# Kernel optimization log

Measured on AMD Instinct MI355X. Metric: run time of the kernel, lower is better.

Reference implementation:

```python
import jax, jax.numpy as jnp
import numpy as np
from jax import lax

EPS = 1e-5
B, C, H, W = 16, 256, 56, 56
HEADS, DIM_K, DIM_U, DIM_OUT = 4, 16, 4, 256
DIM_V = DIM_OUT // HEADS  # 64
R = 15


def setup_inputs() -> dict:
    key = jax.random.key(0)
    ks = jax.random.split(key, 16)
    s = 0.05
    return {
        "x": jax.random.normal(ks[0], (B, C, H, W), jnp.float32),
        "Wq": jax.random.normal(ks[1], (C, HEADS * DIM_K), jnp.float32) * s,
        "Wk": jax.random.normal(ks[2], (C, DIM_U * DIM_K), jnp.float32) * s,
        "Wv": jax.random.normal(ks[3], (C, DIM_U * DIM_V), jnp.float32) * s,
        "pos_w": jax.random.normal(ks[4], (DIM_K, DIM_U, 1, R, R), jnp.float32) * s,
        "pos_b": jax.random.normal(ks[5], (DIM_K,), jnp.float32) * s,
        "gq": jax.random.uniform(ks[6], (HEADS * DIM_K,), jnp.float32),
        "bq": jax.random.normal(ks[7], (HEADS * DIM_K,), jnp.float32) * s,
        "mq": jax.random.normal(ks[8], (HEADS * DIM_K,), jnp.float32) * s,
        "vq": jax.random.uniform(ks[9], (HEADS * DIM_K,), jnp.float32) + 0.5,
        "gv": jax.random.uniform(ks[10], (DIM_U * DIM_V,), jnp.float32),
        "bv": jax.random.normal(ks[11], (DIM_U * DIM_V,), jnp.float32) * s,
        "mv": jax.random.normal(ks[12], (DIM_U * DIM_V,), jnp.float32) * s,
        "vv": jax.random.uniform(ks[13], (DIM_U * DIM_V,), jnp.float32) + 0.5,
    }


def _bn(x, gamma, beta, mean, var):
    # inference-mode BatchNorm over channel dim (axis=1), x: [b,c,h,w]
    inv = gamma / jnp.sqrt(var + EPS)
    return x * inv[None, :, None, None] + (beta - mean * inv)[None, :, None, None]


def reference(x, Wq, Wk, Wv, pos_w, pos_b, gq, bq, mq, vq, gv, bv, mv, vv):
    b, c, hh, ww = x.shape
    n = hh * ww
    h, dk, u, dv = HEADS, DIM_K, DIM_U, DIM_V
    # 1x1 convs (channels_first) == channel matmuls
    q = jnp.einsum('bchw,cd->bdhw', x, Wq)
    k = jnp.einsum('bchw,cd->bdhw', x, Wk)
    v = jnp.einsum('bchw,cd->bdhw', x, Wv)
    q = _bn(q, gq, bq, mq, vq)
    v = _bn(v, gv, bv, mv, vv)
    # rearranges: 'b (h k) hh ww -> b h k (hh ww)', 'b (u k) hh ww -> b u k n', 'b (u v) hh ww -> b u v n'
    q = q.reshape(b, h, dk, n)
    k = k.reshape(b, u, dk, n)
    v = v.reshape(b, u, dv, n)
    k = jax.nn.softmax(k, axis=-1)  # keras Softmax default axis=-1 (positions)
    # content lambda
    Lc = jnp.einsum('bukm,buvm->bkv', k, v)
    Yc = jnp.einsum('bhkn,bkv->bnhv', q, Lc)
    # position lambda: conv3d over (v,hh,ww) with kernel (1,r,r), pad spatial only
    v5 = v.reshape(b, u, dv, hh, ww)  # [N, C=u, D=v, H, W]
    p = R // 2
    Lp = lax.conv_general_dilated(
        v5, pos_w, window_strides=(1, 1, 1),
        padding=[(0, 0), (p, p), (p, p)],
        dimension_numbers=('NCDHW', 'OIDHW', 'NCDHW'))
    Lp = Lp + pos_b[None, :, None, None, None]  # [b, k, v, hh, ww]
    Lp = Lp.reshape(b, dk, dv, n)
    Yp = jnp.einsum('bhkn,bkvn->bnhv', q, Lp)
    Y = Yc + Yp  # [b, n, h, v]
    # 'b (hh ww) h v -> b (h v) hh ww'
    out = Y.reshape(b, hh, ww, h, dv).transpose(0, 3, 4, 1, 2).reshape(b, h * dv, hh, ww)
    return out
```

## Files before the change

kernel.cpp:

```cpp
#include <hip/hip_runtime.h>
#include <cstdint>
#include <cstddef>

#define NB   16
#define NC   256
#define NPIX 3136
#define NW   56
#define EPSV 1e-5f

#define BSTR   (384 * NPIX)
#define OFF_VP (128 * NPIX)
#define VROWD  36
#define VPLANE (56 * VROWD)

#define OFF_AB   0u
#define OFF_BNA  49152u
#define OFF_BNB  49536u
#define OFF_WT   49920u
#define OFF_KS   58112u
#define OFF_LC   59136u
#define OFF_Y    75520u

typedef short bf16x8 __attribute__((ext_vector_type(8)));
typedef float f32x4  __attribute__((ext_vector_type(4)));
typedef float f32x16 __attribute__((ext_vector_type(16)));

__device__ __forceinline__ uint32_t f2bf(float f) {
  uint32_t x = __float_as_uint(f);
  uint32_t r = x + 0x7fffu + ((x >> 16) & 1u);
  return r >> 16;
}
__device__ __forceinline__ uint32_t pk_trunc(float a, float b) {
  return (__float_as_uint(a) >> 16) | (__float_as_uint(b) & 0xffff0000u);
}

__device__ __forceinline__ float fetchW(const float* Wq, const float* Wk,
                                        const float* Wv, int m, int c) {
  if (m < 64)  return Wq[c * 64 + m];
  if (m < 128) return Wk[c * 64 + (m - 64)];
  return Wv[c * 256 + (m - 128)];
}

__global__ void prep_kernel(const float* __restrict__ Wq, const float* __restrict__ Wk,
                            const float* __restrict__ Wv, const float* __restrict__ pos_w,
                            const float* __restrict__ gq, const float* __restrict__ bq,
                            const float* __restrict__ mq, const float* __restrict__ vq,
                            const float* __restrict__ gv, const float* __restrict__ bv,
                            const float* __restrict__ mv, const float* __restrict__ vv,
                            float* __restrict__ ws) {
  int d = blockIdx.x;
  int c = threadIdx.x;
  int i = d * 256 + c;
  if (i < 49152) {
    int dgt = i >> 12, rem = i & 4095;
    int kc = rem >> 8, rem2 = rem & 255;
    int lane = rem2 >> 2, dp = rem2 & 3;
    int m = dgt * 32 + (lane & 31);
    int k0 = kc * 16 + (lane >> 5) * 8 + dp * 2;
    float w0 = fetchW(Wq, Wk, Wv, m, k0);
    float w1 = fetchW(Wq, Wk, Wv, m, k0 + 1);
    ((uint32_t*)(ws + OFF_AB))[i] = f2bf(w0) | (f2bf(w1) << 16);
  }
  if (c == 0) {
    float sa, sb;
    if (d < 64)        { float inv = gq[d] / sqrtf(vq[d] + EPSV); sa = inv; sb = bq[d] - mq[d] * inv; }
    else if (d < 128)  { sa = 1.0f; sb = 0.0f; }
    else               { int j = d - 128; float inv = gv[j] / sqrtf(vv[j] + EPSV); sa = inv; sb = bv[j] - mv[j] * inv; }
    ws[OFF_BNA + d] = sa;
    ws[OFF_BNB + d] = sb;
  }
  if (i < 8192) {
    int chunk = i >> 8, rem = i & 255, lane = rem >> 2, dp = rem & 3;
    int quad = lane >> 4, k = lane & 15;
    int u = chunk >> 3, t = chunk & 7;
    int dh = 2 * t + (quad >> 1);
    int dwb = (quad & 1) * 8 + dp * 2;
    float w0 = (dh < 15 && dwb     < 15) ? pos_w[k * 900 + u * 225 + dh * 15 + dwb]     : 0.0f;
    float w1 = (dh < 15 && dwb + 1 < 15) ? pos_w[k * 900 + u * 225 + dh * 15 + dwb + 1] : 0.0f;
    ((uint32_t*)(ws + OFF_WT))[i] = f2bf(w0) | (f2bf(w1) << 16);
  }
  if (i < 1024) ws[OFF_KS + i] = 0.0f;
  for (int g = i; g < 4096 * 56; g += 98304) {
    int plane = g / 56, r = g - plane * 56;
    int bb = plane >> 8, d2 = plane & 255;
    uint32_t* row = (uint32_t*)(ws + OFF_Y) + (size_t)bb * BSTR + OFF_VP
                    + (size_t)d2 * VPLANE + r * VROWD;
    uint4 z; z.x = 0; z.y = 0; z.z = 0; z.w = 0;
    *(uint4*)(row)      = z;
    *(uint4*)(row + 32) = z;
  }
}

__launch_bounds__(256, 2)
__global__ void qkv_mfma(const float* __restrict__ x, const float* __restrict__ wsc,
                         float* __restrict__ Y) {
  __shared__ uint32_t X[64 * 128];
  __shared__ float BNs[768];
  int tid = threadIdx.x;
  int n0 = blockIdx.x * 64, b = blockIdx.y;
  for (int i = tid; i < 768; i += 256) BNs[i] = wsc[OFF_BNA + i];
  const size_t xb = (size_t)b * NC * NPIX;
#pragma unroll
  for (int it = 0; it < 4; ++it) {
    int n2 = tid & 31;
    int cp4 = it * 8 + (tid >> 5);
    const float* xp = x + xb + (size_t)(cp4 * 8) * NPIX + n0 + n2 * 2;
    float2 ld[8];
#pragma unroll
    for (int j = 0; j < 8; ++j) ld[j] = *(const float2*)(xp + (size_t)j * NPIX);
    uint32_t e0, e1, e2, e3, o0, o1, o2, o3;
    e0 = f2bf(ld[0].x) | (f2bf(ld[1].x) << 16);
    e1 = f2bf(ld[2].x) | (f2bf(ld[3].x) << 16);
    e2 = f2bf(ld[4].x) | (f2bf(ld[5].x) << 16);
    e3 = f2bf(ld[6].x) | (f2bf(ld[7].x) << 16);
    o0 = f2bf(ld[0].y) | (f2bf(ld[1].y) << 16);
    o1 = f2bf(ld[2].y) | (f2bf(ld[3].y) << 16);
    o2 = f2bf(ld[4].y) | (f2bf(ld[5].y) << 16);
    o3 = f2bf(ld[6].y) | (f2bf(ld[7].y) << 16);
    int ne = 2 * n2, no = ne + 1;
    uint4 ve; ve.x = e0; ve.y = e1; ve.z = e2; ve.w = e3;
    uint4 vo; vo.x = o0; vo.y = o1; vo.z = o2; vo.w = o3;
    *(uint4*)(X + ne * 128 + ((cp4 ^ (ne & 31)) << 2)) = ve;
    *(uint4*)(X + no * 128 + ((cp4 ^ (no & 31)) << 2)) = vo;
  }
  __syncthreads();
  int lane = tid & 63, w = tid >> 6;
  int n31 = lane & 31, h5 = lane >> 5;
  f32x16 acc[3][2];
#pragma unroll
  for (int dt = 0; dt < 3; ++dt)
#pragma unroll
    for (int nt = 0; nt < 2; ++nt)
#pragma unroll
      for (int e = 0; e < 16; ++e) acc[dt][nt][e] = 0.0f;
  const uint4* AB = (const uint4*)(wsc + OFF_AB);
#pragma unroll 4
  for (int kc = 0; kc < 16; ++kc) {
    bf16x8 af[3];
#pragma unroll
    for (int dt = 0; dt < 3; ++dt) {
      union { uint4 q; bf16x8 v; } tmp;
      tmp.q = AB[(size_t)(((w * 3 + dt) * 16 + kc)) * 64 + lane];
      af[dt] = tmp.v;
    }
#pragma unroll
    for (int nt = 0; nt < 2; ++nt) {
      union { uint4 q; bf16x8 v; } bu;
      bu.q = *(const uint4*)(X + (nt * 32 + n31) * 128 + (((2 * kc + h5) ^ n31) << 2));
#pragma unroll
      for (int dt = 0; dt < 3; ++dt)
        acc[dt][nt] = __builtin_amdgcn_mfma_f32_32x32x16_bf16(af[dt], bu.v, acc[dt][nt], 0, 0, 0);
    }
  }
#pragma unroll
  for (int dt = 0; dt < 3; ++dt) {
    int dgt = w * 3 + dt;
    float sa[16], sb[16];
#pragma unroll
    for (int g = 0; g < 4; ++g) {
      *(float4*)(sa + g * 4) = *(const float4*)(BNs + dgt * 32 + g * 8 + h5 * 4);
      *(float4*)(sb + g * 4) = *(const float4*)(BNs + 384 + dgt * 32 + g * 8 + h5 * 4);
    }
#pragma unroll
    for (int nt = 0; nt < 2; ++nt) {
      int pix = n0 + nt * 32 + n31;
      if (dgt < 2) {
        uint2* qb2 = (uint2*)(Y + (size_t)b * BSTR);
#pragma unroll
        for (int g = 0; g < 4; ++g) {
          float y0 = fmaf(acc[dt][nt][4 * g + 0], sa[4 * g + 0], sb[4 * g + 0]);
          float y1 = fmaf(acc[dt][nt][4 * g + 1], sa[4 * g + 1], sb[4 * g + 1]);
          float y2 = fmaf(acc[dt][nt][4 * g + 2], sa[4 * g + 2], sb[4 * g + 2]);
          float y3 = fmaf(acc[dt][nt][4 * g + 3], sa[4 * g + 3], sb[4 * g + 3]);
          uint2 val;
          val.x = f2bf(y0) | (f2bf(y1) << 16);
          val.y = f2bf(y2) | (f2bf(y3) << 16);
          qb2[(size_t)(dgt * 8 + 2 * g + h5) * NPIX + pix] = val;
        }
      } else if (dgt < 4) {
#pragma unroll
        for (int g = 0; g < 4; ++g)
#pragma unroll
          for (int ki = 0; ki < 4; ++ki) {
            int d = dgt * 32 + 8 * g + 4 * h5 + ki;
            Y[((size_t)b * 384 + d) * NPIX + pix] =
                fmaf(acc[dt][nt][4 * g + ki], sa[4 * g + ki], sb[4 * g + ki]);
          }
      } else {
        int pr = pix / NW, pc = pix - pr * NW;
        int ridx = pr * 72 + 8 + pc;
        unsigned short* vp = (unsigned short*)(Y + (size_t)b * BSTR + OFF_VP);
#pragma unroll
        for (int g = 0; g < 4; ++g)
#pragma unroll
          for (int ki = 0; ki < 4; ++ki) {
            int d2 = dgt * 32 + 8 * g + 4 * h5 + ki - 128;
            float yv = fmaf(acc[dt][nt][4 * g + ki], sa[4 * g + ki], sb[4 * g + ki]);
            vp[(size_t)d2 * 4032 + ridx] = (unsigned short)f2bf(yv);
          }
      }
    }
  }
}

__launch_bounds__(256)
__global__ void lc_mfma(float* __restrict__ Y, float* __restrict__ ws) {
  __shared__ float R[4096];
  __shared__ float Rs[64];
  int bx = blockIdx.x, u = blockIdx.y, b = blockIdx.z;
  int tid = threadIdx.x;
  int lane = tid & 63, w = tid >> 6;
  int col = lane & 15, quad = lane >> 4;
  int slot = bx * 4 + w;
  const float* krow = Y + ((size_t)(b * 384 + 64 + u * 16 + col)) * NPIX;
  const uint32_t* vpb = (const uint32_t*)(Y + (size_t)b * BSTR + OFF_VP)
                        + (size_t)(u * 64 + col) * VPLANE;
  f32x4 acc[4];
#pragma unroll
  for (int vt = 0; vt < 4; ++vt) acc[vt] = (f32x4){0.f, 0.f, 0.f, 0.f};
  float ssum = 0.0f;
  for (int c = slot; c < 126; c += 64) {
    int p0 = c * 32 + quad * 8;
    int row = p0 / 72;
    int pc = p0 - row * 72;
    bool valid = (unsigned)(pc - 8) < 56u;
    float4 k0, k1;
    if (valid) {
      const float* kp = krow + row * NW + pc - 8;
      k0 = *(const float4*)(kp);
      k1 = *(const float4*)(kp + 4);
    } else {
      k0.x = k0.y = k0.z = k0.w = -1e30f;
      k1 = k0;
    }
    float e0 = __expf(k0.x), e1 = __expf(k0.y), e2 = __expf(k0.z), e3 = __expf(k0.w);
    float e4 = __expf(k1.x), e5 = __expf(k1.y), e6 = __expf(k1.z), e7 = __expf(k1.w);
    ssum += (e0 + e1 + e2 + e3) + (e4 + e5 + e6 + e7);
    union { uint32_t d[4]; bf16x8 v; } kb;
    kb.d[0] = pk_trunc(e0, e1);
    kb.d[1] = pk_trunc(e2, e3);
    kb.d[2] = pk_trunc(e4, e5);
    kb.d[3] = pk_trunc(e6, e7);
    int vdw = c * 16 + quad * 4;
#pragma unroll
    for (int vt = 0; vt < 4; ++vt) {
      union { uint4 q; bf16x8 v; } vb;
      vb.q = *(const uint4*)(vpb + (size_t)(vt * 16) * VPLANE + vdw);
      acc[vt] = __builtin_amdgcn_mfma_f32_16x16x32_bf16(vb.v, kb.v, acc[vt], 0, 0, 0);
    }
  }
  ssum += __shfl_xor(ssum, 16);
  ssum += __shfl_xor(ssum, 32);
#pragma unroll
  for (int vt = 0; vt < 4; ++vt)
#pragma unroll
    for (int r = 0; r < 4; ++r)
      R[w * 1024 + vt * 256 + quad * 64 + r * 16 + col] = acc[vt][r];
  if (lane < 16) Rs[w * 16 + col] = ssum;
  __syncthreads();
  float* P = Y + (size_t)b * BSTR + 32 * NPIX + (size_t)(u * 16 + bx) * 1024;
  float4 s0 = *(const float4*)(R + tid * 4);
  float4 s1 = *(const float4*)(R + 1024 + tid * 4);
  float4 s2 = *(const float4*)(R + 2048 + tid * 4);
  float4 s3 = *(const float4*)(R + 3072 + tid * 4);
  float4 tot;
  tot.x = (s0.x + s1.x) + (s2.x + s3.x);
  tot.y = (s0.y + s1.y) + (s2.y + s3.y);
  tot.z = (s0.z + s1.z) + (s2.z + s3.z);
  tot.w = (s0.w + s1.w) + (s2.w + s3.w);
  *(float4*)(P + tid * 4) = tot;
  if (tid < 16)
    atomicAdd(&ws[OFF_KS + b * 64 + u * 16 + tid],
              (Rs[tid] + Rs[16 + tid]) + (Rs[32 + tid] + Rs[48 + tid]));
}

__global__ void lc_reduce(const float* __restrict__ Y, float* __restrict__ ws) {
  int i = blockIdx.x, b = blockIdx.y;
  int t = threadIdx.x;
  __shared__ float invS[64];
  if (t < 64) invS[t] = 1.0f / ws[OFF_KS + b * 64 + t];
  __syncthreads();
  int idx = i * 256 + t;
  int k = idx & 15;
  const float* P = Y + (size_t)b * BSTR + 32 * NPIX;
  float tot = 0.0f;
#pragma unroll
  for (int u = 0; u < 4; ++u) {
    float su = 0.0f;
#pragma unroll
    for (int s = 0; s < 16; ++s) su += P[(size_t)(u * 16 + s) * 1024 + idx];
    tot += su * invS[u * 16 + k];
  }
  ws[OFF_LC + (b * 16 + k) * 64 + (idx >> 4)] = tot;
}

#define ROWS    29
#define RSTR2   72
#define UPITCH2 2088
#define LDSW2   8352

__launch_bounds__(512, 4)
__global__ void pos_lambda_mfma(const float* __restrict__ Y, const float* __restrict__ wsc,
                                const float* __restrict__ pos_b, float* __restrict__ out) {
  __shared__ __attribute__((aligned(16))) uint32_t S[LDSW2];
  int v = blockIdx.x, b = blockIdx.y, band = blockIdx.z;
  int rb = band * 14;
  int tid = threadIdx.x;
  const uint32_t* vpad = (const uint32_t*)(Y + (size_t)b * BSTR + OFF_VP);
  for (int ii = tid; ii < 1044; ii += 512) {
    int u = ii / 261;
    int rem = ii - u * 261;
    int row = rem / 9;
    int j3 = rem - row * 9;
    int gr = rb + row - 7;
    uint32_t d0 = 0, d1 = 0, d2 = 0, d3 = 0, d4 = 0;
    if ((unsigned)gr < (unsigned)NW) {
      const uint32_t* pr32 = vpad + (size_t)(u * 64 + v) * VPLANE + gr * VROWD + 4 * j3;
      d0 = pr32[0]; d1 = pr32[1]; d2 = pr32[2]; d3 = pr32[3]; d4 = pr32[4];
    }
    uint32_t* dst = S + u * UPITCH2 + row * RSTR2 + 8 * j3;
    uint4 w0, w1;
    w0.x = __builtin_amdgcn_alignbit(d1, d0, 16);  w0.y = d1;
    w0.z = __builtin_amdgcn_alignbit(d2, d1, 16);  w0.w = d2;
    w1.x = __builtin_amdgcn_alignbit(d3, d2, 16);  w1.y = d3;
    w1.z = __builtin_amdgcn_alignbit(d4, d3, 16);  w1.w = d4;
    *(uint4*)(dst)     = w0;
    *(uint4*)(dst + 4) = w1;
  }
  __syncthreads();
  int lane = tid & 63, wid = tid >> 6;
  int quad = lane >> 4, n = lane & 15;
  int dhp = quad >> 1;
  int ct = wid & 3, p = wid >> 2;
  int cb = (ct == 3) ? 40 : ct * 16;
  int sb = cb + n + (quad & 1) * 8;
  int abase = (p + dhp) * RSTR2 + sb;
  const uint4* wt = (const uint4*)(wsc + OFF_WT);
  float lcq[4];
#pragma unroll
  for (int r = 0; r < 4; ++r) {
    int k = quad * 4 + r;
    lcq[r] = wsc[OFF_LC + (b * 16 + k) * 64 + v] + pos_b[k];
  }
  f32x4 acc[7];
#pragma unroll
  for (int q = 0; q < 7; ++q) {
    acc[q][0] = lcq[0]; acc[q][1] = lcq[1]; acc[q][2] = lcq[2]; acc[q][3] = lcq[3];
  }
#pragma unroll 1
  for (int u = 0; u < 4; ++u) {
    bf16x8 wf[8];
#pragma unroll
    for (int t = 0; t < 8; ++t) {
      union { uint4 q; bf16x8 v; } tmp;
      tmp.q = wt[(u * 8 + t) * 64 + lane];
      wf[t] = tmp.v;
    }
    int au = u * UPITCH2 + abase;
#pragma unroll
    for (int PP = 0; PP < 14; ++PP) {
      int a = au + PP * (2 * RSTR2);
      union { uint32_t u4[4]; bf16x8 v8; } bu;
      bu.u4[0] = S[a];     bu.u4[1] = S[a + 2];
      bu.u4[2] = S[a + 4]; bu.u4[3] = S[a + 6];
#pragma unroll
      for (int t = 0; t < 8; ++t) {
        int q = PP - t;
        if (q >= 0 && q < 7)
          acc[q] = __builtin_amdgcn_mfma_f32_16x16x32_bf16(wf[t], bu.v8, acc[q], 0, 0, 0);
      }
    }
  }
  const uint2* qb2 = (const uint2*)(Y + (size_t)b * BSTR);
#pragma unroll
  for (int q = 0; q < 7; ++q) {
    int rr = rb + p + 2 * q;
    int pix = rr * NW + cb + n;
    float m0 = acc[q][0], m1 = acc[q][1];
    float m2 = acc[q][2], m3 = acc[q][3];
    float pp[4];
#pragma unroll
    for (int j = 0; j < 4; ++j) {
      int h = quad ^ j;
      uint2 qd = qb2[(h * 4 + quad) * NPIX + pix];
      float q0 = __uint_as_float(qd.x << 16);
      float q1 = __uint_as_float(qd.x & 0xffff0000u);
      float q2 = __uint_as_float(qd.y << 16);
      float q3 = __uint_as_float(qd.y & 0xffff0000u);
      pp[j] = fmaf(q0, m0, fmaf(q1, m1, fmaf(q2, m2, q3 * m3)));
    }
    float t0 = pp[0] + __shfl_xor(pp[1], 16);
    float t2 = pp[2] + __shfl_xor(pp[3], 16);
    float y  = t0 + __shfl_xor(t2, 32);
    out[((size_t)(b * 256 + quad * 64 + v)) * NPIX + pix] = y;
  }
}

extern "C" void kernel_launch(void* const* d_in, const int* in_sizes, int n_in,
                              void* d_out, int out_size, void* d_ws, size_t ws_size,
                              hipStream_t stream) {
  const float* x     = (const float*)d_in[0];
  const float* Wq    = (const float*)d_in[1];
  const float* Wk    = (const float*)d_in[2];
  const float* Wv    = (const float*)d_in[3];
  const float* pos_w = (const float*)d_in[4];
  const float* pos_b = (const float*)d_in[5];
  const float* gq    = (const float*)d_in[6];
  const float* bq    = (const float*)d_in[7];
  const float* mq    = (const float*)d_in[8];
  const float* vq    = (const float*)d_in[9];
  const float* gv    = (const float*)d_in[10];
  const float* bv    = (const float*)d_in[11];
  const float* mv    = (const float*)d_in[12];
  const float* vv    = (const float*)d_in[13];
  float* ws  = (float*)d_ws;
  float* out = (float*)d_out;
  float* Y   = ws + OFF_Y;

  prep_kernel<<<dim3(384), 256, 0, stream>>>(Wq, Wk, Wv, pos_w, gq, bq, mq, vq,
                                             gv, bv, mv, vv, ws);
  qkv_mfma<<<dim3(49, 16), 256, 0, stream>>>(x, ws, Y);
  lc_mfma<<<dim3(16, 4, 16), 256, 0, stream>>>(Y, ws);
  lc_reduce<<<dim3(4, 16), 256, 0, stream>>>(Y, ws);
  pos_lambda_mfma<<<dim3(64, 16, 4), 512, 0, stream>>>(Y, ws, pos_b, out);
}
```

Measured before the change: 261.1 us.

## Split LDS tile into parity planes, skip padded-row MFMAs and duplicate stores

The position-lambda kernel now stages each input row in shared memory as two planes: an aligned copy and a half-word-shifted copy. Each B fragment can then be read from four consecutive words instead of four words at stride two. The MFMA loop also skips row pairs that fall entirely in the zero padding at the top and bottom bands. The overlapping last column tile no longer writes its duplicated pixels. The global load becomes a single 16-byte read, and the shared-memory footprint grows slightly, which could press on occupancy at four blocks per CU.

Result: slower. 291.6 us (+11.7%).

```diff
diff --git a/kernel.cpp b/kernel.cpp
--- a/kernel.cpp
+++ b/kernel.cpp
@@ -295,14 +295,15 @@
 }
 
 #define ROWS    29
-#define RSTR2   72
-#define UPITCH2 2088
-#define LDSW2   8352
+#define RSTR3   80
+#define P1OFF   44
+#define UPITCH3 2320
+#define LDSW3   9280
 
 __launch_bounds__(512, 4)
 __global__ void pos_lambda_mfma(const float* __restrict__ Y, const float* __restrict__ wsc,
                                 const float* __restrict__ pos_b, float* __restrict__ out) {
-  __shared__ __attribute__((aligned(16))) uint32_t S[LDSW2];
+  __shared__ __attribute__((aligned(16))) uint32_t S[LDSW3];
   int v = blockIdx.x, b = blockIdx.y, band = blockIdx.z;
   int rb = band * 14;
   int tid = threadIdx.x;
@@ -311,21 +312,24 @@
     int u = ii / 261;
     int rem = ii - u * 261;
     int row = rem / 9;
-    int j3 = rem - row * 9;
+    int j = rem - row * 9;
     int gr = rb + row - 7;
     uint32_t d0 = 0, d1 = 0, d2 = 0, d3 = 0, d4 = 0;
     if ((unsigned)gr < (unsigned)NW) {
-      const uint32_t* pr32 = vpad + (size_t)(u * 64 + v) * VPLANE + gr * VROWD + 4 * j3;
-      d0 = pr32[0]; d1 = pr32[1]; d2 = pr32[2]; d3 = pr32[3]; d4 = pr32[4];
-    }
-    uint32_t* dst = S + u * UPITCH2 + row * RSTR2 + 8 * j3;
-    uint4 w0, w1;
-    w0.x = __builtin_amdgcn_alignbit(d1, d0, 16);  w0.y = d1;
-    w0.z = __builtin_amdgcn_alignbit(d2, d1, 16);  w0.w = d2;
-    w1.x = __builtin_amdgcn_alignbit(d3, d2, 16);  w1.y = d3;
-    w1.z = __builtin_amdgcn_alignbit(d4, d3, 16);  w1.w = d4;
-    *(uint4*)(dst)     = w0;
-    *(uint4*)(dst + 4) = w1;
+      const uint32_t* pr = vpad + (size_t)(u * 64 + v) * VPLANE + gr * VROWD + 4 * j;
+      uint4 q4 = *(const uint4*)pr;
+      d0 = q4.x; d1 = q4.y; d2 = q4.z; d3 = q4.w;
+      d4 = pr[4];
+    }
+    uint32_t* dst = S + u * UPITCH3 + row * RSTR3 + 4 * j;
+    uint4 a4; a4.x = d0; a4.y = d1; a4.z = d2; a4.w = d3;
+    *(uint4*)(dst) = a4;
+    uint4 b4;
+    b4.x = __builtin_amdgcn_alignbit(d1, d0, 16);
+    b4.y = __builtin_amdgcn_alignbit(d2, d1, 16);
+    b4.z = __builtin_amdgcn_alignbit(d3, d2, 16);
+    b4.w = __builtin_amdgcn_alignbit(d4, d3, 16);
+    *(uint4*)(dst + P1OFF) = b4;
   }
   __syncthreads();
   int lane = tid & 63, wid = tid >> 6;
@@ -333,8 +337,11 @@
   int dhp = quad >> 1;
   int ct = wid & 3, p = wid >> 2;
   int cb = (ct == 3) ? 40 : ct * 16;
-  int sb = cb + n + (quad & 1) * 8;
-  int abase = (p + dhp) * RSTR2 + sb;
+  int s = cb + n + ((quad & 1) << 3) + 1;
+  int par = s & 1, sidx = s >> 1;
+  int base = (p + dhp) * RSTR3 + (par ? P1OFF : 0) + sidx;
+  int lo = (7 - rb) > 0 ? (7 - rb) : 0;
+  int hi = (63 - rb) < ROWS ? (63 - rb) : ROWS;
   const uint4* wt = (const uint4*)(wsc + OFF_WT);
   float lcq[4];
 #pragma unroll
@@ -356,13 +363,16 @@
       tmp.q = wt[(u * 8 + t) * 64 + lane];
       wf[t] = tmp.v;
     }
-    int au = u * UPITCH2 + abase;
+    const uint32_t* Sp = S + u * UPITCH3 + base;
 #pragma unroll
     for (int PP = 0; PP < 14; ++PP) {
-      int a = au + PP * (2 * RSTR2);
+      int r0 = p + 2 * PP;
+      if (r0 + 1 < lo || r0 >= hi) continue;
       union { uint32_t u4[4]; bf16x8 v8; } bu;
-      bu.u4[0] = S[a];     bu.u4[1] = S[a + 2];
-      bu.u4[2] = S[a + 4]; bu.u4[3] = S[a + 6];
+      bu.u4[0] = Sp[PP * 160];
+      bu.u4[1] = Sp[PP * 160 + 1];
+      bu.u4[2] = Sp[PP * 160 + 2];
+      bu.u4[3] = Sp[PP * 160 + 3];
 #pragma unroll
       for (int t = 0; t < 8; ++t) {
         int q = PP - t;
@@ -371,28 +381,31 @@
       }
     }
   }
-  const uint2* qb2 = (const uint2*)(Y + (size_t)b * BSTR);
-#pragma unroll
-  for (int q = 0; q < 7; ++q) {
-    int rr = rb + p + 2 * q;
-    int pix = rr * NW + cb + n;
-    float m0 = acc[q][0], m1 = acc[q][1];
-    float m2 = acc[q][2], m3 = acc[q][3];
-    float pp[4];
-#pragma unroll
-    for (int j = 0; j < 4; ++j) {
-      int h = quad ^ j;
-      uint2 qd = qb2[(h * 4 + quad) * NPIX + pix];
-      float q0 = __uint_as_float(qd.x << 16);
-      float q1 = __uint_as_float(qd.x & 0xffff0000u);
-      float q2 = __uint_as_float(qd.y << 16);
-      float q3 = __uint_as_float(qd.y & 0xffff0000u);
-      pp[j] = fmaf(q0, m0, fmaf(q1, m1, fmaf(q2, m2, q3 * m3)));
-    }
-    float t0 = pp[0] + __shfl_xor(pp[1], 16);
-    float t2 = pp[2] + __shfl_xor(pp[3], 16);
-    float y  = t0 + __shfl_xor(t2, 32);
-    out[((size_t)(b * 256 + quad * 64 + v)) * NPIX + pix] = y;
+  bool dup = (ct == 3) && (n < 8);
+  if (!dup) {
+    const uint2* qb2 = (const uint2*)(Y + (size_t)b * BSTR);
+#pragma unroll
+    for (int q = 0; q < 7; ++q) {
+      int rr = rb + p + 2 * q;
+      int pix = rr * NW + cb + n;
+      float m0 = acc[q][0], m1 = acc[q][1];
+      float m2 = acc[q][2], m3 = acc[q][3];
+      float pp[4];
+#pragma unroll
+      for (int j = 0; j < 4; ++j) {
+        int h = quad ^ j;
+        uint2 qd = qb2[(h * 4 + quad) * NPIX + pix];
+        float q0 = __uint_as_float(qd.x << 16);
+        float q1 = __uint_as_float(qd.x & 0xffff0000u);
+        float q2 = __uint_as_float(qd.y << 16);
+        float q3 = __uint_as_float(qd.y & 0xffff0000u);
+        pp[j] = fmaf(q0, m0, fmaf(q1, m1, fmaf(q2, m2, q3 * m3)));
+      }
+      float t0 = pp[0] + __shfl_xor(pp[1], 16);
+      float t2 = pp[2] + __shfl_xor(pp[3], 16);
+      float y  = t0 + __shfl_xor(t2, 32);
+      out[((size_t)(b * 256 + quad * 64 + v)) * NPIX + pix] = y;
+    }
   }
 }
 
```
